# Optimization experiments

Hardware: AMD Instinct MI355X
Metric: run time of the kernel (lower is better)

Reference implementation:

```python
import jax, jax.numpy as jnp
import numpy as np

NUM_HEADS = 8
NUM_LEVELS = 4
NUM_POINTS = 8
SPATIAL_SHAPES = np.array([[92, 160], [46, 80], [23, 40], [12, 20]], dtype=np.int64)


def _bilinear_sample(val_hw, loc, Hl, Wl):
    """val_hw: (bs, heads, H*W, d); loc: (bs, nq, heads, P, 2) in [0,1].
    Matches torch grid_sample(bilinear, zeros padding, align_corners=False)
    applied to grid = 2*loc - 1, i.e. pixel coords x = loc_x*W - 0.5.
    Returns (bs, heads, nq, P, d)."""
    x = loc[..., 0] * Wl - 0.5
    y = loc[..., 1] * Hl - 0.5
    x0 = jnp.floor(x)
    y0 = jnp.floor(y)
    wx = (x - x0).transpose(0, 2, 1, 3)  # (bs, heads, nq, P)
    wy = (y - y0).transpose(0, 2, 1, 3)
    x0i = x0.astype(jnp.int32).transpose(0, 2, 1, 3)
    y0i = y0.astype(jnp.int32).transpose(0, 2, 1, 3)

    def gather(ix, iy):
        valid = ((ix >= 0) & (ix < Wl) & (iy >= 0) & (iy < Hl)).astype(val_hw.dtype)
        idx = jnp.clip(iy, 0, Hl - 1) * Wl + jnp.clip(ix, 0, Wl - 1)  # (bs,heads,nq,P)
        b, h, nq, P = idx.shape
        g = jnp.take_along_axis(val_hw, idx.reshape(b, h, nq * P, 1), axis=2)
        return g.reshape(b, h, nq, P, -1) * valid[..., None]

    return (gather(x0i, y0i) * ((1 - wx) * (1 - wy))[..., None]
            + gather(x0i + 1, y0i) * (wx * (1 - wy))[..., None]
            + gather(x0i, y0i + 1) * ((1 - wx) * wy)[..., None]
            + gather(x0i + 1, y0i + 1) * (wx * wy)[..., None])


def setup_inputs() -> dict:
    key = jax.random.key(0)
    ks = jax.random.split(key, 10)
    C = 256
    bs, nq = 2, 10000
    nv = int((SPATIAL_SHAPES[:, 0] * SPATIAL_SHAPES[:, 1]).sum())  # 19560
    s = 1.0 / np.sqrt(C)
    return {
        "query": jax.random.normal(ks[0], (bs, nq, C), dtype=jnp.float32),
        "value": jax.random.normal(ks[1], (bs, nv, C), dtype=jnp.float32),
        "reference_points": jax.random.uniform(ks[2], (bs, nq, 4, 2), dtype=jnp.float32),
        "spatial_shapes": SPATIAL_SHAPES,
        "W_value": jax.random.normal(ks[3], (C, C), dtype=jnp.float32) * s,
        "b_value": jnp.zeros((C,), dtype=jnp.float32),
        "W_off": jax.random.normal(ks[4], (C, NUM_HEADS * NUM_LEVELS * NUM_POINTS * 2), dtype=jnp.float32) * 0.01,
        "b_off": jax.random.normal(ks[5], (NUM_HEADS * NUM_LEVELS * NUM_POINTS * 2,), dtype=jnp.float32) * 0.1,
        "W_attn": jax.random.normal(ks[6], (C, NUM_HEADS * NUM_LEVELS * NUM_POINTS), dtype=jnp.float32) * s,
        "b_attn": jnp.zeros((NUM_HEADS * NUM_LEVELS * NUM_POINTS,), dtype=jnp.float32),
    }


def reference(query, value, reference_points, spatial_shapes,
              W_value, b_value, W_off, b_off, W_attn, b_attn):
    bs, nq, C = query.shape
    NH, NL, NP = NUM_HEADS, NUM_LEVELS, NUM_POINTS
    d = C // NH
    Z = reference_points.shape[2]  # num_Z_anchors
    shapes_np = np.asarray(spatial_shapes)  # static host-side shapes

    # value / offset / attention projections
    v = (value @ W_value + b_value).reshape(bs, -1, NH, d)
    off = (query @ W_off + b_off).reshape(bs, nq, NH, NL, NP, 2)
    attn = jax.nn.softmax((query @ W_attn + b_attn).reshape(bs, nq, NH, NL * NP), axis=-1)
    attn = attn.reshape(bs, nq, NH, NL, NP)

    # normalize offsets by (W, H) per level and add to reference points
    norm = jnp.stack([spatial_shapes[:, 1], spatial_shapes[:, 0]], -1).astype(query.dtype)  # (NL, 2)
    off = off / norm[None, None, None, :, None, :]
    off = off.reshape(bs, nq, NH, NL, NP // Z, Z, 2)
    loc = reference_points[:, :, None, None, None, :, :] + off  # (bs,nq,NH,NL,NP//Z,Z,2)
    loc = loc.reshape(bs, nq, NH, NL, NP, 2)

    out = jnp.zeros((bs, NH, nq, d), dtype=query.dtype)
    start = 0
    for l in range(NL):
        Hl, Wl = int(shapes_np[l, 0]), int(shapes_np[l, 1])
        v_l = v[:, start:start + Hl * Wl].transpose(0, 2, 1, 3)  # (bs, NH, H*W, d)
        start += Hl * Wl
        sampled = _bilinear_sample(v_l, loc[:, :, :, l], Hl, Wl)  # (bs,NH,nq,NP,d)
        out = out + jnp.einsum('bhqpd,bqhp->bhqd', sampled, attn[:, :, :, l])
    return out.transpose(0, 2, 1, 3).reshape(bs, nq, NH * d)
```

## Files before the change

kernel.cpp:

```cpp
#include <hip/hip_runtime.h>
#include <math.h>

#define NH 8
#define NL 4
#define NP 8
#define CDIM 256
#define NQ 10000
#define BS 2
#define NV 19560

__constant__ int LVL_H[NL]     = {92, 46, 23, 12};
__constant__ int LVL_W[NL]     = {160, 80, 40, 20};
__constant__ int LVL_START[NL] = {0, 14720, 18400, 19320};

typedef __attribute__((ext_vector_type(8))) short short8;
typedef __attribute__((ext_vector_type(4))) float f32x4;
typedef __attribute__((ext_vector_type(2))) _Float16 half2v;
typedef __attribute__((ext_vector_type(4))) _Float16 half4v;

__device__ __forceinline__ unsigned short f2bf(float f) {
    unsigned int u = __float_as_uint(f);
    u += 0x7fffu + ((u >> 16) & 1u);
    return (unsigned short)(u >> 16);
}

__device__ __forceinline__ unsigned f2h_dup(float f) {
    const unsigned short h = __builtin_bit_cast(unsigned short, (_Float16)f);
    return (unsigned)h | ((unsigned)h << 16);
}

__global__ __launch_bounds__(256) void prep_all(
    const float* __restrict__ query,
    const float* __restrict__ Wv,
    const float* __restrict__ Woff, const float* __restrict__ boff,
    const float* __restrict__ Wattn, const float* __restrict__ battn,
    unsigned short* __restrict__ querybf,
    unsigned short* __restrict__ BvalT, unsigned short* __restrict__ BcatT,
    float* __restrict__ biascat)
{
    const int bid = blockIdx.x;
    const int t   = threadIdx.x;
    if (bid < 5000) {
        const int i = bid * 256 + t;
        const float4 f = ((const float4*)query)[i];
        ushort4 o;
        o.x = f2bf(f.x); o.y = f2bf(f.y); o.z = f2bf(f.z); o.w = f2bf(f.w);
        ((ushort4*)querybf)[i] = o;
    } else {
        const int n = bid - 5000;
        if (n < 256) {
            BvalT[n * 256 + t] = f2bf(Wv[t * 256 + n]);
        } else if (n < 1024) {
            const int m = n - 256;
            const float v = (m < 512) ? Woff[t * 512 + m]
                                      : Wattn[t * 256 + (m - 512)];
            BcatT[m * 256 + t] = f2bf(v);
        } else {
            #pragma unroll
            for (int s = 0; s < 3; s++) {
                const int i = s * 256 + t;
                biascat[i] = (i < 512) ? boff[i] : battn[i - 512];
            }
        }
    }
}

#define AST 130
__global__ __launch_bounds__(256) void gemm_all(
    const float* __restrict__ valueF,
    const unsigned short* __restrict__ BvalT,
    const float* __restrict__ b_value, _Float16* __restrict__ vproj,
    const unsigned short* __restrict__ querybf,
    const unsigned short* __restrict__ BcatT,
    const float* __restrict__ biascat, _Float16* __restrict__ offcat)
{
    __shared__ short8 Al[4 * AST];
    __shared__ short8 Bl[4 * AST];

    const int bid = blockIdx.x;
    const bool modeV = bid < 612;

    const unsigned short* Bt;
    const float* bias;
    int M, N, rowBase, colBase;
    if (modeV) {
        Bt = BvalT; bias = b_value;
        M = BS * NV; N = 256;
        rowBase = (bid >> 1) * 128; colBase = (bid & 1) * 128;
    } else {
        const int b2 = bid - 612;
        Bt = BcatT; bias = biascat;
        M = BS * NQ; N = 768;
        rowBase = (b2 / 6) * 128; colBase = (b2 % 6) * 128;
    }

    const int t = threadIdx.x;
    const int w  = t >> 6;
    const int l  = t & 63;
    const int wm = (w >> 1) * 64;
    const int wn = (w & 1) * 64;
    const int row16 = l & 15;
    const int kg    = l >> 4;

    const int sr = t >> 1;
    const int sh = t & 1;

    f32x4 acc[4][4] = {};

    for (int k0 = 0; k0 < 256; k0 += 32) {
        {
            const int grow = rowBase + sr;
            short8 v0 = {}, v1 = {};
            if (modeV) {
                if (grow < M) {
                    const float* ap = valueF + (size_t)grow * 256 + k0 + sh * 16;
                    float va[16];
                    #pragma unroll
                    for (int jj = 0; jj < 4; jj++) {
                        const float4 f = *(const float4*)(ap + jj * 4);
                        va[jj*4+0]=f.x; va[jj*4+1]=f.y;
                        va[jj*4+2]=f.z; va[jj*4+3]=f.w;
                    }
                    #pragma unroll
                    for (int e = 0; e < 8; e++) {
                        v0[e] = (short)f2bf(va[e]);
                        v1[e] = (short)f2bf(va[8 + e]);
                    }
                }
            } else {
                if (grow < M) {
                    const unsigned short* ap =
                        querybf + (size_t)grow * 256 + k0 + sh * 16;
                    v0 = *(const short8*)ap;
                    v1 = *(const short8*)(ap + 8);
                }
            }
            Al[(sh * 2 + 0) * AST + sr] = v0;
            Al[(sh * 2 + 1) * AST + sr] = v1;
        }
        {
            const unsigned short* bp = Bt + (size_t)(colBase + sr) * 256 + k0 + sh * 16;
            Bl[(sh * 2 + 0) * AST + sr] = *(const short8*)bp;
            Bl[(sh * 2 + 1) * AST + sr] = *(const short8*)(bp + 8);
        }
        __syncthreads();

        short8 af[4], bfr[4];
        #pragma unroll
        for (int i = 0; i < 4; i++) af[i] = Al[kg * AST + wm + i * 16 + row16];
        #pragma unroll
        for (int j = 0; j < 4; j++) bfr[j] = Bl[kg * AST + wn + j * 16 + row16];
        #pragma unroll
        for (int i = 0; i < 4; i++)
            #pragma unroll
            for (int j = 0; j < 4; j++)
                acc[i][j] = __builtin_amdgcn_mfma_f32_16x16x32_bf16(
                    bfr[j], af[i], acc[i][j], 0, 0, 0);
        __syncthreads();
    }

    const int m16 = l & 15;
    const int q4  = (l >> 4) * 4;
    #pragma unroll
    for (int i = 0; i < 4; i++) {
        const int row = rowBase + wm + i * 16 + m16;
        if (row >= M) continue;
        #pragma unroll
        for (int j = 0; j < 4; j++) {
            const int col0 = colBase + wn + j * 16 + q4;
            const float4 bv = *(const float4*)&bias[col0];
            half4v o;
            o[0] = (_Float16)(acc[i][j][0] + bv.x);
            o[1] = (_Float16)(acc[i][j][1] + bv.y);
            o[2] = (_Float16)(acc[i][j][2] + bv.z);
            o[3] = (_Float16)(acc[i][j][3] + bv.w);
            _Float16* dst;
            if (modeV) {
                const int b   = (row >= NV) ? 1 : 0;
                const int pix = row - b * NV;
                const int h   = col0 >> 5;
                const int ch  = col0 & 31;
                dst = vproj + ((size_t)(b * NH + h) * NV + pix) * 32 + ch;
            } else {
                dst = offcat + (size_t)row * 768 + col0;
            }
            *(half4v*)dst = o;
        }
    }
}

__global__ __launch_bounds__(256, 8) void sample_kernel(
    const _Float16* __restrict__ vproj,
    const _Float16* __restrict__ offcat,
    const float* __restrict__ refpts,
    float* __restrict__ out)
{
    const int bid = blockIdx.x;
    const int h   = bid & 7;
    const int g   = bid >> 3;
    const int b   = g & 1;
    const int q0  = (g >> 1) * 8;
    const int t   = threadIdx.x;

    __shared__ uint2 desc[8 * 136];

    const int qi = t >> 5, j = t & 31;
    const int qrow = b * NQ + q0 + qi;

    {
        const int lv = j >> 3, p = j & 7;

        const float logit = (float)offcat[(size_t)qrow * 768 + 512 + h * 32 + j];
        const float e = __expf(logit);
        float ssum = e;
        #pragma unroll
        for (int s = 16; s > 0; s >>= 1) ssum += __shfl_xor(ssum, s, 32);
        const float aw = e / ssum;

        const int Wl = LVL_W[lv], Hl = LVL_H[lv], st = LVL_START[lv];
        const uint oxy = *(const uint*)(offcat + (size_t)qrow * 768 + h * 64 + j * 2);
        const float offx = (float)__builtin_bit_cast(half2v, oxy)[0];
        const float offy = (float)__builtin_bit_cast(half2v, oxy)[1];

        const int z = p & 3;
        const float rx = refpts[((size_t)qrow * 4 + z) * 2];
        const float ry = refpts[((size_t)qrow * 4 + z) * 2 + 1];

        const float x = fmaf(rx, (float)Wl, offx) - 0.5f;
        const float y = fmaf(ry, (float)Hl, offy) - 0.5f;
        const float x0f = floorf(x), y0f = floorf(y);
        const float wx = x - x0f, wy = y - y0f;
        const int x0 = (int)x0f, y0 = (int)y0f;

        const int xb = min(max(x0, 0), Wl - 2);
        const float wl = (x0 >= 0 && x0 < Wl)          ? (1.f - wx) : 0.f;
        const float wr = (x0 + 1 >= 0 && x0 + 1 < Wl)  ? wx         : 0.f;
        const float wA = (x0 == xb) ? wl : ((x0 + 1 == xb) ? wr : 0.f);
        const float wB = (x0 == xb) ? wr : ((x0 == xb + 1) ? wl : 0.f);

        #pragma unroll
        for (int r = 0; r < 2; r++) {
            const int yy = y0 + r;
            const float rwv = (yy >= 0 && yy < Hl)
                            ? (r ? wy : (1.f - wy)) * aw : 0.f;
            const int iy = min(max(yy, 0), Hl - 1);
            const unsigned base = (unsigned)((st + iy * Wl + xb) * 64);
            uint4 dd;
            dd.x = base;      dd.y = f2h_dup(wA * rwv);
            dd.z = base + 64; dd.w = f2h_dup(wB * rwv);
            *(uint4*)&desc[qi * 136 + (j * 2 + r) * 2] = dd;
        }
    }
    __syncthreads();

    const int lane = t & 31;
    const int grp  = lane >> 3;
    const int pix  = (lane >> 2) & 1;
    const int chq  = lane & 3;

    const char* slab = (const char*)(vproj + (size_t)(b * NH + h) * NV * 32);
    const unsigned laneoff = (unsigned)(chq * 16);
    const uint* dqw = (const uint*)&desc[qi * 136 + grp * 2 + pix];

    half2v a0 = {}, a1 = {}, a2 = {}, a3 = {};
    #pragma unroll
    for (int half = 0; half < 2; half++) {
        unsigned addr[8];
        #pragma unroll
        for (int u = 0; u < 8; u++)
            addr[u] = dqw[(half * 8 + u) * 16] + laneoff;
        uint4 v[8];
        #pragma unroll
        for (int u = 0; u < 8; u++)
            v[u] = *(const uint4*)(slab + addr[u]);
        #pragma unroll
        for (int u = 0; u < 8; u++) {
            const half2v wv = __builtin_bit_cast(half2v,
                                  dqw[(half * 8 + u) * 16 + 1]);
            a0 += wv * __builtin_bit_cast(half2v, v[u].x);
            a1 += wv * __builtin_bit_cast(half2v, v[u].y);
            a2 += wv * __builtin_bit_cast(half2v, v[u].z);
            a3 += wv * __builtin_bit_cast(half2v, v[u].w);
        }
    }

    #pragma unroll
    for (int s = 4; s <= 16; s <<= 1) {
        a0 += __builtin_bit_cast(half2v,
              __shfl_xor(__builtin_bit_cast(unsigned, a0), s, 32));
        a1 += __builtin_bit_cast(half2v,
              __shfl_xor(__builtin_bit_cast(unsigned, a1), s, 32));
        a2 += __builtin_bit_cast(half2v,
              __shfl_xor(__builtin_bit_cast(unsigned, a2), s, 32));
        a3 += __builtin_bit_cast(half2v,
              __shfl_xor(__builtin_bit_cast(unsigned, a3), s, 32));
    }

    if ((lane & 0x1C) == 0) {
        float* op = out + (size_t)qrow * 256 + h * 32 + chq * 8;
        *(float4*)op = make_float4((float)a0[0], (float)a0[1],
                                   (float)a1[0], (float)a1[1]);
        *(float4*)(op + 4) = make_float4((float)a2[0], (float)a2[1],
                                         (float)a3[0], (float)a3[1]);
    }
}

extern "C" void kernel_launch(void* const* d_in, const int* in_sizes, int n_in,
                              void* d_out, int out_size, void* d_ws, size_t ws_size,
                              hipStream_t stream)
{
    const float* query   = (const float*)d_in[0];
    const float* value   = (const float*)d_in[1];
    const float* refpts  = (const float*)d_in[2];
    const float* W_value = (const float*)d_in[4];
    const float* b_value = (const float*)d_in[5];
    const float* W_off   = (const float*)d_in[6];
    const float* b_off   = (const float*)d_in[7];
    const float* W_attn  = (const float*)d_in[8];
    const float* b_attn  = (const float*)d_in[9];

    char* ws = (char*)d_ws;
    _Float16*       vproj   = (_Float16*)(ws);
    unsigned short* querybf = (unsigned short*)(ws + 20029440);
    _Float16*       offcat  = (_Float16*)(ws + 30269440);
    unsigned short* BvalT   = (unsigned short*)(ws + 60989440);
    unsigned short* BcatT   = (unsigned short*)(ws + 61120512);
    float*          biascat = (float*)(ws + 61513728);

    const dim3 blk(256);

    prep_all<<<dim3(6025), blk, 0, stream>>>(
        query, W_value, W_off, b_off, W_attn, b_attn,
        querybf, BvalT, BcatT, biascat);

    gemm_all<<<dim3(1554), blk, 0, stream>>>(
        value, BvalT, b_value, vproj,
        querybf, BcatT, biascat, offcat);

    sample_kernel<<<dim3(BS * NQ), blk, 0, stream>>>(
        vproj, offcat, refpts, (float*)d_out);
}
```

Measured before the change: 213.1 us.

## Use direct global-to-LDS loads with swizzle in GEMM and repack sampler descriptors

The GEMM tile loads for the bf16 operands now use global_load_lds to write straight into shared memory, with an XOR-style rotated layout in place of the padded one, and out-of-range rows are clamped instead of zero-filled. The fp32 value path still converts in registers, just with the new layout. In the sampling kernel the descriptor table is reorganised so each lane reads its addresses and weights as 16-byte vectors rather than scalar LDS reads. The aim is fewer register round-trips and LDS instructions, at the cost of relying on intrinsic semantics and a more intricate indexing scheme.

```diff
diff --git a/kernel.cpp b/kernel.cpp
--- a/kernel.cpp
+++ b/kernel.cpp
@@ -27,6 +27,12 @@
 __device__ __forceinline__ unsigned f2h_dup(float f) {
     const unsigned short h = __builtin_bit_cast(unsigned short, (_Float16)f);
     return (unsigned)h | ((unsigned)h << 16);
+}
+
+__device__ __forceinline__ void glds16(const void* g, void* l) {
+    __builtin_amdgcn_global_load_lds(
+        (const __attribute__((address_space(1))) unsigned*)g,
+        (__attribute__((address_space(3))) unsigned*)l, 16, 0, 0);
 }
 
 __global__ __launch_bounds__(256) void prep_all(
@@ -65,7 +71,6 @@
     }
 }
 
-#define AST 130
 __global__ __launch_bounds__(256) void gemm_all(
     const float* __restrict__ valueF,
     const unsigned short* __restrict__ BvalT,
@@ -74,8 +79,8 @@
     const unsigned short* __restrict__ BcatT,
     const float* __restrict__ biascat, _Float16* __restrict__ offcat)
 {
-    __shared__ short8 Al[4 * AST];
-    __shared__ short8 Bl[4 * AST];
+    __shared__ short8 Asl[512];
+    __shared__ short8 Bsl[512];
 
     const int bid = blockIdx.x;
     const bool modeV = bid < 612;
@@ -102,54 +107,57 @@
     const int row16 = l & 15;
     const int kg    = l >> 4;
 
-    const int sr = t >> 1;
-    const int sh = t & 1;
+    const int r0 = t >> 2;
+    const int m_ = t & 3;
+    const int cs = (m_ - (r0 >> 1)) & 3;
+
+    short8* aw0 = &Asl[(w << 6)];
+    short8* aw1 = &Asl[256 + (w << 6)];
+    short8* bw0 = &Bsl[(w << 6)];
+    short8* bw1 = &Bsl[256 + (w << 6)];
+
+    const int arow0 = min(rowBase + r0, M - 1);
+    const int arow1 = min(rowBase + r0 + 64, M - 1);
+    const int brow0 = colBase + r0;
+    const int brow1 = brow0 + 64;
 
     f32x4 acc[4][4] = {};
 
     for (int k0 = 0; k0 < 256; k0 += 32) {
-        {
-            const int grow = rowBase + sr;
-            short8 v0 = {}, v1 = {};
-            if (modeV) {
-                if (grow < M) {
-                    const float* ap = valueF + (size_t)grow * 256 + k0 + sh * 16;
-                    float va[16];
-                    #pragma unroll
-                    for (int jj = 0; jj < 4; jj++) {
-                        const float4 f = *(const float4*)(ap + jj * 4);
-                        va[jj*4+0]=f.x; va[jj*4+1]=f.y;
-                        va[jj*4+2]=f.z; va[jj*4+3]=f.w;
-                    }
-                    #pragma unroll
-                    for (int e = 0; e < 8; e++) {
-                        v0[e] = (short)f2bf(va[e]);
-                        v1[e] = (short)f2bf(va[8 + e]);
-                    }
-                }
-            } else {
-                if (grow < M) {
-                    const unsigned short* ap =
-                        querybf + (size_t)grow * 256 + k0 + sh * 16;
-                    v0 = *(const short8*)ap;
-                    v1 = *(const short8*)(ap + 8);
-                }
+        const int kc = k0 + cs * 8;
+        glds16(Bt + (size_t)brow0 * 256 + kc, bw0);
+        glds16(Bt + (size_t)brow1 * 256 + kc, bw1);
+        if (modeV) {
+            #pragma unroll
+            for (int jj = 0; jj < 2; jj++) {
+                const int ar = jj ? arow1 : arow0;
+                const float* ap = valueF + (size_t)ar * 256 + kc;
+                const float4 f0 = *(const float4*)ap;
+                const float4 f1 = *(const float4*)(ap + 4);
+                short8 v;
+                v[0] = (short)f2bf(f0.x); v[1] = (short)f2bf(f0.y);
+                v[2] = (short)f2bf(f0.z); v[3] = (short)f2bf(f0.w);
+                v[4] = (short)f2bf(f1.x); v[5] = (short)f2bf(f1.y);
+                v[6] = (short)f2bf(f1.z); v[7] = (short)f2bf(f1.w);
+                Asl[jj * 256 + t] = v;
             }
-            Al[(sh * 2 + 0) * AST + sr] = v0;
-            Al[(sh * 2 + 1) * AST + sr] = v1;
-        }
-        {
-            const unsigned short* bp = Bt + (size_t)(colBase + sr) * 256 + k0 + sh * 16;
-            Bl[(sh * 2 + 0) * AST + sr] = *(const short8*)bp;
-            Bl[(sh * 2 + 1) * AST + sr] = *(const short8*)(bp + 8);
+        } else {
+            glds16(querybf + (size_t)arow0 * 256 + kc, aw0);
+            glds16(querybf + (size_t)arow1 * 256 + kc, aw1);
         }
         __syncthreads();
 
         short8 af[4], bfr[4];
         #pragma unroll
-        for (int i = 0; i < 4; i++) af[i] = Al[kg * AST + wm + i * 16 + row16];
-        #pragma unroll
-        for (int j = 0; j < 4; j++) bfr[j] = Bl[kg * AST + wn + j * 16 + row16];
+        for (int i = 0; i < 4; i++) {
+            const int r = wm + i * 16 + row16;
+            af[i] = Asl[r * 4 + ((kg + (r >> 1)) & 3)];
+        }
+        #pragma unroll
+        for (int j = 0; j < 4; j++) {
+            const int r = wn + j * 16 + row16;
+            bfr[j] = Bsl[r * 4 + ((kg + (r >> 1)) & 3)];
+        }
         #pragma unroll
         for (int i = 0; i < 4; i++)
             #pragma unroll
@@ -202,7 +210,7 @@
     const int q0  = (g >> 1) * 8;
     const int t   = threadIdx.x;
 
-    __shared__ uint2 desc[8 * 136];
+    __shared__ uint2 desc[8 * 144];
 
     const int qi = t >> 5, j = t & 31;
     const int qrow = b * NQ + q0 + qi;
@@ -237,6 +245,9 @@
         const float wr = (x0 + 1 >= 0 && x0 + 1 < Wl)  ? wx         : 0.f;
         const float wA = (x0 == xb) ? wl : ((x0 + 1 == xb) ? wr : 0.f);
         const float wB = (x0 == xb) ? wr : ((x0 == xb + 1) ? wl : 0.f);
+
+        const int i16 = j >> 1;
+        const int gA0 = qi * 144 + (((j & 1) * 2) * 2) * 18 + i16;
 
         #pragma unroll
         for (int r = 0; r < 2; r++) {
@@ -245,10 +256,9 @@
                             ? (r ? wy : (1.f - wy)) * aw : 0.f;
             const int iy = min(max(yy, 0), Hl - 1);
             const unsigned base = (unsigned)((st + iy * Wl + xb) * 64);
-            uint4 dd;
-            dd.x = base;      dd.y = f2h_dup(wA * rwv);
-            dd.z = base + 64; dd.w = f2h_dup(wB * rwv);
-            *(uint4*)&desc[qi * 136 + (j * 2 + r) * 2] = dd;
+            const int gb = gA0 + r * 2 * 18;
+            desc[gb]      = make_uint2(base,      f2h_dup(wA * rwv));
+            desc[gb + 18] = make_uint2(base + 64, f2h_dup(wB * rwv));
         }
     }
     __syncthreads();
@@ -260,27 +270,32 @@
 
     const char* slab = (const char*)(vproj + (size_t)(b * NH + h) * NV * 32);
     const unsigned laneoff = (unsigned)(chq * 16);
-    const uint* dqw = (const uint*)&desc[qi * 136 + grp * 2 + pix];
+    const uint4* dp = (const uint4*)&desc[qi * 144 + (grp * 2 + pix) * 18];
 
     half2v a0 = {}, a1 = {}, a2 = {}, a3 = {};
     #pragma unroll
     for (int half = 0; half < 2; half++) {
-        unsigned addr[8];
-        #pragma unroll
-        for (int u = 0; u < 8; u++)
-            addr[u] = dqw[(half * 8 + u) * 16] + laneoff;
+        uint4 d4[4];
+        #pragma unroll
+        for (int u2 = 0; u2 < 4; u2++) d4[u2] = dp[half * 4 + u2];
         uint4 v[8];
         #pragma unroll
-        for (int u = 0; u < 8; u++)
-            v[u] = *(const uint4*)(slab + addr[u]);
-        #pragma unroll
-        for (int u = 0; u < 8; u++) {
-            const half2v wv = __builtin_bit_cast(half2v,
-                                  dqw[(half * 8 + u) * 16 + 1]);
-            a0 += wv * __builtin_bit_cast(half2v, v[u].x);
-            a1 += wv * __builtin_bit_cast(half2v, v[u].y);
-            a2 += wv * __builtin_bit_cast(half2v, v[u].z);
-            a3 += wv * __builtin_bit_cast(half2v, v[u].w);
+        for (int u2 = 0; u2 < 4; u2++) {
+            v[u2 * 2]     = *(const uint4*)(slab + (d4[u2].x + laneoff));
+            v[u2 * 2 + 1] = *(const uint4*)(slab + (d4[u2].z + laneoff));
+        }
+        #pragma unroll
+        for (int u2 = 0; u2 < 4; u2++) {
+            const half2v w0 = __builtin_bit_cast(half2v, d4[u2].y);
+            a0 += w0 * __builtin_bit_cast(half2v, v[u2 * 2].x);
+            a1 += w0 * __builtin_bit_cast(half2v, v[u2 * 2].y);
+            a2 += w0 * __builtin_bit_cast(half2v, v[u2 * 2].z);
+            a3 += w0 * __builtin_bit_cast(half2v, v[u2 * 2].w);
+            const half2v w1 = __builtin_bit_cast(half2v, d4[u2].w);
+            a0 += w1 * __builtin_bit_cast(half2v, v[u2 * 2 + 1].x);
+            a1 += w1 * __builtin_bit_cast(half2v, v[u2 * 2 + 1].y);
+            a2 += w1 * __builtin_bit_cast(half2v, v[u2 * 2 + 1].z);
+            a3 += w1 * __builtin_bit_cast(half2v, v[u2 * 2 + 1].w);
         }
     }
 
```

After: 200.6 us. 1.06x faster.
